# Performance work log

Hardware: AMD Instinct MI355X
Metric: run time of the kernel (lower is better)

The kernel has to match this reference:

```python
import jax, jax.numpy as jnp
import numpy as np
import math

D_MODEL = 1024
N_HEADS = 16
D_K = D_MODEL // N_HEADS
ROPE_BASE = 10000.0


def rope_cos_sin(seq_len, d_k, base=ROPE_BASE, dtype=jnp.float32):
    inv_freq = 1.0 / base ** (jnp.arange(0, d_k, 2, dtype=dtype) / d_k)  # [d_k/2]
    pos = jnp.arange(seq_len, dtype=dtype)
    freqs = jnp.outer(pos, inv_freq)  # [T, d_k/2]
    return jnp.cos(freqs), jnp.sin(freqs)


def apply_rope(x, cos, sin):
    # x: [B, H, T, d_k]; cos/sin: [T, d_k/2]
    x1 = x[..., 0::2]
    x2 = x[..., 1::2]
    c = cos[None, None]
    s = sin[None, None]
    r1 = x1 * c - x2 * s
    r2 = x1 * s + x2 * c
    return jnp.stack([r1, r2], axis=-1).reshape(x.shape)


def setup_inputs() -> dict:
    key = jax.random.key(0)
    ks = jax.random.split(key, 7)
    B, T = 2, 2048
    scale = 1.0 / math.sqrt(D_MODEL)
    return {
        "query": jax.random.normal(ks[0], (B, T, D_MODEL), jnp.float32),
        "key": jax.random.normal(ks[1], (B, T, D_MODEL), jnp.float32),
        "value": jax.random.normal(ks[2], (B, T, D_MODEL), jnp.float32),
        "Wq": jax.random.normal(ks[3], (D_MODEL, D_MODEL), jnp.float32) * scale,
        "Wk": jax.random.normal(ks[4], (D_MODEL, D_MODEL), jnp.float32) * scale,
        "Wv": jax.random.normal(ks[5], (D_MODEL, D_MODEL), jnp.float32) * scale,
        "Wo": jax.random.normal(ks[6], (D_MODEL, D_MODEL), jnp.float32) * scale,
    }


def reference(query, key, value, Wq, Wk, Wv, Wo):
    B, Tq, _ = query.shape
    Tk = key.shape[1]
    # nn.Linear: x @ W.T
    Q = (query @ Wq.T).reshape(B, Tq, N_HEADS, D_K).transpose(0, 2, 1, 3)
    K = (key @ Wk.T).reshape(B, Tk, N_HEADS, D_K).transpose(0, 2, 1, 3)
    V = (value @ Wv.T).reshape(B, Tk, N_HEADS, D_K).transpose(0, 2, 1, 3)
    cos_q, sin_q = rope_cos_sin(Tq, D_K)
    cos_k, sin_k = rope_cos_sin(Tk, D_K)
    Q = apply_rope(Q, cos_q, sin_q)
    K = apply_rope(K, cos_k, sin_k)
    scores = jnp.einsum("bhqd,bhkd->bhqk", Q, K) / math.sqrt(D_K)
    attn = jax.nn.softmax(scores, axis=-1)
    out = jnp.einsum("bhqk,bhkd->bhqd", attn, V)
    out = out.transpose(0, 2, 1, 3).reshape(B, Tq, D_MODEL)
    return out @ Wo.T
```

## Files before the change

### kernel.cpp

```cpp
#include <hip/hip_runtime.h>
#include <hip/hip_bf16.h>
#include <cstdint>

typedef unsigned short u16;
typedef __attribute__((ext_vector_type(4))) float fl4;
typedef __attribute__((ext_vector_type(2))) float fl2;
typedef __attribute__((ext_vector_type(4))) unsigned short u16x4;
typedef __attribute__((ext_vector_type(8))) unsigned short u16x8;
typedef __attribute__((ext_vector_type(2))) unsigned int u32x2;
typedef __attribute__((ext_vector_type(8))) __bf16 bf16x8;
typedef __attribute__((ext_vector_type(4))) float f32x4;

#define MKE 4194304
#define NKE 1048576

static __device__ __forceinline__ u16 f2bf(float x) {
  unsigned int u = __builtin_bit_cast(unsigned int, x);
  u += 0x7fffu + ((u >> 16) & 1u);
  return (u16)(u >> 16);
}

static __device__ __forceinline__ unsigned int cvtpk(float a, float b) {
  unsigned int r;
  asm("v_cvt_pk_bf16_f32 %0, %1, %2" : "=v"(r) : "v"(a), "v"(b));
  return r;
}

static __device__ __forceinline__ f32x4 mfma16(bf16x8 a, bf16x8 b, f32x4 c) {
  return __builtin_amdgcn_mfma_f32_16x16x32_bf16(a, b, c, 0, 0, 0);
}

static __device__ __forceinline__ void gload_lds16(const void* g, void* l) {
  __builtin_amdgcn_global_load_lds((const __attribute__((address_space(1))) void*)g,
                                   (__attribute__((address_space(3))) void*)l,
                                   16, 0, 0);
}

__global__ __launch_bounds__(256) void k_prep(const float* __restrict__ q,
                                              const float* __restrict__ k,
                                              const float* __restrict__ v,
                                              const float* __restrict__ wq,
                                              const float* __restrict__ wk,
                                              const float* __restrict__ wv,
                                              const float* __restrict__ wo,
                                              u16* __restrict__ ws,
                                              float* __restrict__ tab) {
  const int bid = blockIdx.x;
  if (bid >= 16384) {
    const int idx = (bid - 16384) * 256 + threadIdx.x;
    const int t = idx >> 5, i = idx & 31;
    const float ang = (float)t * exp2f(-0.4152410118609203f * (float)i);
    float sn, cs;
    sincosf(ang, &sn, &cs);
    reinterpret_cast<fl2*>(tab)[idx] = (fl2){cs, sn};
    return;
  }
  const int i = bid * 256 + threadIdx.x;
  const float* src;
  u16* dst;
  int loc;
  if (i < 3 * 1048576) {
    const int seg = i >> 20;
    loc = i & 1048575;
    src = seg == 0 ? q : (seg == 1 ? k : v);
    dst = ws + (size_t)seg * MKE;
  } else {
    const int j = i - 3 * 1048576;
    const int seg = j >> 18;
    loc = j & 262143;
    src = seg == 0 ? wq : (seg == 1 ? wk : (seg == 2 ? wv : wo));
    dst = ws + 3 * (size_t)MKE + (size_t)seg * NKE;
  }
  fl4 val = reinterpret_cast<const fl4*>(src)[loc];
  u16x4 o;
  o[0] = f2bf(val[0]); o[1] = f2bf(val[1]); o[2] = f2bf(val[2]); o[3] = f2bf(val[3]);
  reinterpret_cast<u16x4*>(dst)[loc] = o;
}

__global__ __launch_bounds__(256) void k_gemm_qkv(
    const u16* __restrict__ aq, const u16* __restrict__ ak, const u16* __restrict__ av,
    const u16* __restrict__ bq, const u16* __restrict__ bk, const u16* __restrict__ bv,
    u16* __restrict__ cq, u16* __restrict__ ck, u16* __restrict__ cv,
    const fl2* __restrict__ tab) {
  constexpr int K = 1024;
  __shared__ __align__(16) u16 smem[16384];
  u16* sA = smem;
  u16* sB = smem + 8192;
  const int z = blockIdx.z;
  const u16* A  = z == 0 ? aq : (z == 1 ? ak : av);
  const u16* Bw = z == 0 ? bq : (z == 1 ? bk : bv);
  u16* C        = z == 0 ? cq : (z == 1 ? ck : cv);
  const float scale = (z == 0) ? 0.18033688011112042f : 1.0f;

  const int tid = threadIdx.x;
  const int w = tid >> 6, lane = tid & 63;
  const int wm = w >> 1, wn = w & 1;
  const int trow = blockIdx.y << 7, tcol = blockIdx.x << 7;
  const int l15 = lane & 15, l4 = lane >> 4;
  const int srow = lane >> 3;
  const int scol = ((lane & 7) ^ srow) << 3;

  f32x4 acc[4][4];
#pragma unroll
  for (int m = 0; m < 4; ++m)
#pragma unroll
    for (int n = 0; n < 4; ++n) acc[m][n] = (f32x4){0.f, 0.f, 0.f, 0.f};

  for (int k0 = 0; k0 < K; k0 += 64) {
#pragma unroll
    for (int c = 0; c < 4; ++c) {
      const int g = c * 4 + w;
      const int row = g * 8 + srow;
      gload_lds16(A + (size_t)(trow + row) * K + (k0 + scol), (void*)(sA + g * 512));
      gload_lds16(Bw + (size_t)(tcol + row) * K + (k0 + scol), (void*)(sB + g * 512));
    }
    __syncthreads();
#pragma unroll
    for (int kc = 0; kc < 2; ++kc) {
      const int kb = (kc * 32 + l4 * 8) * 2;
      bf16x8 af[4], bfr[4];
#pragma unroll
      for (int m = 0; m < 4; ++m) {
        const int r = wm * 64 + m * 16 + l15;
        af[m] = *reinterpret_cast<const bf16x8*>(
            reinterpret_cast<const char*>(sA) + r * 128 + (kb ^ ((r & 7) << 4)));
      }
#pragma unroll
      for (int n = 0; n < 4; ++n) {
        const int r = wn * 64 + n * 16 + l15;
        bfr[n] = *reinterpret_cast<const bf16x8*>(
            reinterpret_cast<const char*>(sB) + r * 128 + (kb ^ ((r & 7) << 4)));
      }
      __builtin_amdgcn_s_setprio(1);
#pragma unroll
      for (int m = 0; m < 4; ++m)
#pragma unroll
        for (int n = 0; n < 4; ++n)
          acc[m][n] = mfma16(af[m], bfr[n], acc[m][n]);
      __builtin_amdgcn_s_setprio(0);
    }
    __syncthreads();
  }

  if (z < 2) {
#pragma unroll
    for (int m = 0; m < 4; ++m) {
#pragma unroll
      for (int n = 0; n < 4; ++n) {
#pragma unroll
        for (int r = 0; r < 4; ++r) {
          const float vsc = acc[m][n][r] * scale;
          const int row = trow + wm * 64 + m * 16 + l4 * 4 + r;
          const int col = tcol + wn * 64 + n * 16 + l15;
          const int b = row >> 11, t = row & 2047;
          const int h = col >> 6, d = col & 63;
          const float partner = __shfl_xor(vsc, 1);
          const fl2 cs = tab[t * 32 + (d >> 1)];
          const float outv =
              (d & 1) ? (partner * cs.y + vsc * cs.x) : (vsc * cs.x - partner * cs.y);
          C[((size_t)((b << 4) + h) * 2048 + t) * 64 + d] = f2bf(outv);
        }
      }
    }
  } else {
#pragma unroll
    for (int m = 0; m < 4; ++m)
#pragma unroll
      for (int n = 0; n < 4; ++n)
#pragma unroll
        for (int r = 0; r < 4; ++r) {
          const int c = wn * 64 + n * 16 + l15;
          const int rl = wm * 64 + m * 16 + l4 * 4 + r;
          smem[c * 128 + (rl ^ ((c & 15) * 8))] = f2bf(acc[m][n][r]);
        }
    __syncthreads();
    const int bq = trow >> 11;
    const int tb = trow & 2047;
#pragma unroll
    for (int j = 0; j < 8; ++j) {
      const int flat = (tid + j * 256) * 8;
      const int c = flat >> 7, r0 = flat & 127;
      u16x8 vv = *reinterpret_cast<const u16x8*>(smem + c * 128 + (r0 ^ ((c & 15) * 8)));
      const int col = tcol + c;
      u16* dst = C + ((size_t)((bq << 4) + (col >> 6)) * 64 + (col & 63)) * 2048 + tb + r0;
      *reinterpret_cast<u16x8*>(dst) = vv;
    }
  }
}

__global__ __launch_bounds__(256) void k_gemm_o(const u16* __restrict__ A,
                                                const u16* __restrict__ Bw,
                                                float* __restrict__ C) {
  constexpr int K = 1024, N = 1024;
  __shared__ __align__(16) u16 sA[2][128 * 64];
  __shared__ __align__(16) u16 sB[2][64 * 64];
  const int tid = threadIdx.x;
  const int w = tid >> 6, lane = tid & 63;
  const int wm = w >> 1, wn = w & 1;
  const int trow = blockIdx.y << 7, tcol = blockIdx.x << 6;
  const int l15 = lane & 15, l4 = lane >> 4;
  const int srow = lane >> 3;
  const int scol = ((lane & 7) ^ srow) << 3;

  f32x4 acc[4][2];
#pragma unroll
  for (int m = 0; m < 4; ++m)
#pragma unroll
    for (int n = 0; n < 2; ++n) acc[m][n] = (f32x4){0.f, 0.f, 0.f, 0.f};

  auto stage = [&](int k0, int buf) {
#pragma unroll
    for (int c = 0; c < 4; ++c) {
      const int g = c * 4 + w;
      const int row = g * 8 + srow;
      gload_lds16(A + (size_t)(trow + row) * K + (k0 + scol), (void*)(sA[buf] + g * 512));
    }
#pragma unroll
    for (int c = 0; c < 2; ++c) {
      const int g = c * 4 + w;
      const int row = g * 8 + srow;
      gload_lds16(Bw + (size_t)(tcol + row) * K + (k0 + scol), (void*)(sB[buf] + g * 512));
    }
  };

  stage(0, 0);
  __syncthreads();

  for (int t = 0; t < 16; ++t) {
    const int buf = t & 1;
    if (t + 1 < 16) stage((t + 1) * 64, buf ^ 1);
#pragma unroll
    for (int kc = 0; kc < 2; ++kc) {
      const int kb = (kc * 32 + l4 * 8) * 2;
      bf16x8 af[4], bfr[2];
#pragma unroll
      for (int m = 0; m < 4; ++m) {
        const int r = wm * 64 + m * 16 + l15;
        af[m] = *reinterpret_cast<const bf16x8*>(
            reinterpret_cast<const char*>(sA[buf]) + r * 128 + (kb ^ ((r & 7) << 4)));
      }
#pragma unroll
      for (int n = 0; n < 2; ++n) {
        const int r = wn * 32 + n * 16 + l15;
        bfr[n] = *reinterpret_cast<const bf16x8*>(
            reinterpret_cast<const char*>(sB[buf]) + r * 128 + (kb ^ ((r & 7) << 4)));
      }
      __builtin_amdgcn_s_setprio(1);
#pragma unroll
      for (int m = 0; m < 4; ++m)
#pragma unroll
        for (int n = 0; n < 2; ++n)
          acc[m][n] = mfma16(af[m], bfr[n], acc[m][n]);
      __builtin_amdgcn_s_setprio(0);
    }
    __syncthreads();
  }

#pragma unroll
  for (int m = 0; m < 4; ++m)
#pragma unroll
    for (int n = 0; n < 2; ++n)
#pragma unroll
      for (int r = 0; r < 4; ++r) {
        const int row = trow + wm * 64 + m * 16 + l4 * 4 + r;
        const int col = tcol + wn * 32 + n * 16 + l15;
        C[(size_t)row * N + col] = acc[m][n][r];
      }
}

__global__ __launch_bounds__(256) void k_attn(const u16* __restrict__ Q,
                                              const u16* __restrict__ Kh,
                                              const u16* __restrict__ Vt,
                                              u16* __restrict__ Oout) {
  __shared__ __align__(16) char lds[40960];
  const int tid = threadIdx.x;
  const int w = tid >> 6, lane = tid & 63;
  const int l15 = lane & 15, l4 = lane >> 4;
  const int nb = blockIdx.x;
  const int xcd = nb & 7, idx = nb >> 3;
  const int bh = xcd * 4 + (idx >> 5);
  const int q0 = (idx & 31) << 6;

  const u16* Qg = Q + (size_t)bh * (2048 * 64);
  const u16* Kg = Kh + (size_t)bh * (2048 * 64);
  const u16* Vg = Vt + (size_t)bh * (64 * 2048);

  const int swz = (l15 & 7) << 4;
  const int rk0 = l15 * 128 + ((l4 * 16) ^ swz);
  const int rk1 = rk0 ^ 64;
  const int pbase = 32768 + w * 2048 + l15 * 128;
  int pwv[4];
#pragma unroll
  for (int nn = 0; nn < 4; ++nn) pwv[nn] = pbase + (((nn * 32) | (l4 * 8)) ^ swz);
  const int rp0 = pbase + ((l4 * 16) ^ swz);
  const int rp1 = rp0 ^ 64;
  const int wst = w * 1024;

  const int srow8 = lane >> 3;
  const int scol = ((lane & 7) ^ srow8) << 3;
  const u16* gK0 = Kg + (size_t)(w * 8 + srow8) * 64 + scol;
  const u16* gK1 = gK0 + 2048;
  const u16* gV0 = Vg + (size_t)(w * 8 + srow8) * 2048 + scol;
  const u16* gV1 = gV0 + 65536;

  bf16x8 qf0, qf1;
  {
    const u16* qp = Qg + (size_t)(q0 + w * 16 + l15) * 64 + l4 * 8;
    qf0 = *reinterpret_cast<const bf16x8*>(qp);
    qf1 = *reinterpret_cast<const bf16x8*>(qp + 32);
  }

  f32x4 o[4];
#pragma unroll
  for (int nn = 0; nn < 4; ++nn) o[nn] = (f32x4){0.f, 0.f, 0.f, 0.f};
  float lrun = 0.f;

  gload_lds16(gK0, lds + wst);
  gload_lds16(gK1, lds + wst + 4096);
  gload_lds16(gV0, lds + 16384 + wst);
  gload_lds16(gV1, lds + 16384 + wst + 4096);
  gK0 += 4096; gK1 += 4096; gV0 += 64; gV1 += 64;
  __syncthreads();

#define ATTN_STEP(BUFOFF, PREF, POFF)                                            \
  {                                                                              \
    if (PREF) {                                                                  \
      gload_lds16(gK0, lds + (POFF) + wst);                                      \
      gload_lds16(gK1, lds + (POFF) + wst + 4096);                               \
      gload_lds16(gV0, lds + 16384 + (POFF) + wst);                              \
      gload_lds16(gV1, lds + 16384 + (POFF) + wst + 4096);                       \
      gK0 += 4096; gK1 += 4096; gV0 += 64; gV1 += 64;                            \
    }                                                                            \
    f32x4 s[4];                                                                  \
    s[0] = (f32x4){0.f, 0.f, 0.f, 0.f}; s[1] = (f32x4){0.f, 0.f, 0.f, 0.f};      \
    s[2] = (f32x4){0.f, 0.f, 0.f, 0.f}; s[3] = (f32x4){0.f, 0.f, 0.f, 0.f};      \
    __builtin_amdgcn_s_setprio(1);                                               \
    _Pragma("unroll")                                                            \
    for (int nn = 0; nn < 4; ++nn) {                                             \
      bf16x8 kf = *(const bf16x8*)(lds + (BUFOFF) + rk0 + nn * 2048);            \
      s[nn] = mfma16(kf, qf0, s[nn]);                                            \
    }                                                                            \
    _Pragma("unroll")                                                            \
    for (int nn = 0; nn < 4; ++nn) {                                             \
      bf16x8 kf = *(const bf16x8*)(lds + (BUFOFF) + rk1 + nn * 2048);            \
      s[nn] = mfma16(kf, qf1, s[nn]);                                            \
    }                                                                            \
    __builtin_amdgcn_s_setprio(0);                                               \
    float pp[4][4];                                                              \
    _Pragma("unroll")                                                            \
    for (int nn = 0; nn < 4; ++nn) {                                             \
      pp[nn][0] = __builtin_amdgcn_exp2f(s[nn][0]);                              \
      pp[nn][1] = __builtin_amdgcn_exp2f(s[nn][1]);                              \
      pp[nn][2] = __builtin_amdgcn_exp2f(s[nn][2]);                              \
      pp[nn][3] = __builtin_amdgcn_exp2f(s[nn][3]);                              \
    }                                                                            \
    _Pragma("unroll")                                                            \
    for (int nn = 0; nn < 4; ++nn) {                                             \
      u32x2 pk;                                                                  \
      pk[0] = cvtpk(pp[nn][0], pp[nn][1]);                                       \
      pk[1] = cvtpk(pp[nn][2], pp[nn][3]);                                       \
      *(u32x2*)(lds + pwv[nn]) = pk;                                             \
    }                                                                            \
    float rs = ((pp[0][0] + pp[0][1]) + (pp[0][2] + pp[0][3])) +                 \
               ((pp[1][0] + pp[1][1]) + (pp[1][2] + pp[1][3])) +                 \
               ((pp[2][0] + pp[2][1]) + (pp[2][2] + pp[2][3])) +                 \
               ((pp[3][0] + pp[3][1]) + (pp[3][2] + pp[3][3]));                  \
    rs += __shfl_xor(rs, 16);                                                    \
    rs += __shfl_xor(rs, 32);                                                    \
    lrun += rs;                                                                  \
    __builtin_amdgcn_s_setprio(1);                                               \
    _Pragma("unroll")                                                            \
    for (int kc = 0; kc < 2; ++kc) {                                             \
      const bf16x8 pf = *(const bf16x8*)(lds + (kc ? rp1 : rp0));                \
      const int rkk = kc ? rk1 : rk0;                                            \
      _Pragma("unroll")                                                          \
      for (int nn = 0; nn < 4; ++nn) {                                           \
        bf16x8 vf = *(const bf16x8*)(lds + 16384 + (BUFOFF) + rkk + nn * 2048);  \
        o[nn] = mfma16(pf, vf, o[nn]);                                           \
      }                                                                          \
    }                                                                            \
    __builtin_amdgcn_s_setprio(0);                                               \
    __syncthreads();                                                             \
  }

  for (int cc = 0; cc < 16; ++cc) {
    ATTN_STEP(0, 1, 8192)
    ATTN_STEP(8192, (cc != 15), 0)
  }
#undef ATTN_STEP

  const int b = bh >> 4, h = bh & 15;
  float lr[4];
#pragma unroll
  for (int r = 0; r < 4; ++r)
    lr[r] = 1.f / __shfl(lrun, (lane & 48) | (l4 * 4 + r));
#pragma unroll
  for (int nn = 0; nn < 4; ++nn)
#pragma unroll
    for (int r = 0; r < 4; ++r) {
      const int t = q0 + w * 16 + l4 * 4 + r;
      const int d = nn * 16 + l15;
      Oout[((size_t)(b * 2048 + t)) * 1024 + h * 64 + d] = f2bf(o[nn][r] * lr[r]);
    }
}

extern "C" void kernel_launch(void* const* d_in, const int* in_sizes, int n_in,
                              void* d_out, int out_size, void* d_ws, size_t ws_size,
                              hipStream_t stream) {
  const float* q  = (const float*)d_in[0];
  const float* k  = (const float*)d_in[1];
  const float* v  = (const float*)d_in[2];
  const float* wq = (const float*)d_in[3];
  const float* wk = (const float*)d_in[4];
  const float* wv = (const float*)d_in[5];
  const float* wo = (const float*)d_in[6];

  u16* ws = (u16*)d_ws;
  u16* Xq  = ws;
  u16* Xk  = Xq + MKE;
  u16* Xv  = Xk + MKE;
  u16* Wqb = Xv + MKE;
  u16* Wkb = Wqb + NKE;
  u16* Wvb = Wkb + NKE;
  u16* Wob = Wvb + NKE;
  u16* Qr  = Wob + NKE;
  u16* Kr  = Qr + MKE;
  u16* Vtm = Kr + MKE;
  u16* Vtr = Vtm + MKE;
  u16* AO  = Vtr + MKE;
  float* tab = (float*)AO;

  k_prep<<<16640, 256, 0, stream>>>(q, k, v, wq, wk, wv, wo, ws, tab);
  k_gemm_qkv<<<dim3(8, 32, 3), 256, 0, stream>>>(Xq, Xk, Xv, Wqb, Wkb, Wvb,
                                                 Qr, Kr, Vtr, (const fl2*)tab);
  k_attn<<<1024, 256, 0, stream>>>(Qr, Kr, Vtr, AO);
  k_gemm_o<<<dim3(16, 32), 256, 0, stream>>>(AO, Wob, (float*)d_out);
}
```

Measured before the change: 135.9 us.

## Process two 16-row query tiles per wave in attention kernel

```diff
diff --git a/kernel.cpp b/kernel.cpp
--- a/kernel.cpp
+++ b/kernel.cpp
@@ -272,14 +272,14 @@
                                               const u16* __restrict__ Kh,
                                               const u16* __restrict__ Vt,
                                               u16* __restrict__ Oout) {
-  __shared__ __align__(16) char lds[40960];
+  __shared__ __align__(16) char lds[49152];
   const int tid = threadIdx.x;
   const int w = tid >> 6, lane = tid & 63;
   const int l15 = lane & 15, l4 = lane >> 4;
   const int nb = blockIdx.x;
   const int xcd = nb & 7, idx = nb >> 3;
-  const int bh = xcd * 4 + (idx >> 5);
-  const int q0 = (idx & 31) << 6;
+  const int bh = xcd * 4 + (idx >> 4);
+  const int q0 = (idx & 15) << 7;
 
   const u16* Qg = Q + (size_t)bh * (2048 * 64);
   const u16* Kg = Kh + (size_t)bh * (2048 * 64);
@@ -288,12 +288,12 @@
   const int swz = (l15 & 7) << 4;
   const int rk0 = l15 * 128 + ((l4 * 16) ^ swz);
   const int rk1 = rk0 ^ 64;
-  const int pbase = 32768 + w * 2048 + l15 * 128;
-  int pwv[4];
-#pragma unroll
-  for (int nn = 0; nn < 4; ++nn) pwv[nn] = pbase + (((nn * 32) | (l4 * 8)) ^ swz);
-  const int rp0 = pbase + ((l4 * 16) ^ swz);
-  const int rp1 = rp0 ^ 64;
+  const int pbase = 32768 + w * 4096 + l15 * 128;
+  int pwvA[4];
+#pragma unroll
+  for (int nn = 0; nn < 4; ++nn) pwvA[nn] = pbase + (((nn * 32) | (l4 * 8)) ^ swz);
+  const int rpA0 = pbase + ((l4 * 16) ^ swz);
+  const int rpA1 = rpA0 ^ 64;
   const int wst = w * 1024;
 
   const int srow8 = lane >> 3;
@@ -303,17 +303,23 @@
   const u16* gV0 = Vg + (size_t)(w * 8 + srow8) * 2048 + scol;
   const u16* gV1 = gV0 + 65536;
 
-  bf16x8 qf0, qf1;
+  bf16x8 qf0, qf1, qf2, qf3;
   {
-    const u16* qp = Qg + (size_t)(q0 + w * 16 + l15) * 64 + l4 * 8;
-    qf0 = *reinterpret_cast<const bf16x8*>(qp);
-    qf1 = *reinterpret_cast<const bf16x8*>(qp + 32);
-  }
-
-  f32x4 o[4];
-#pragma unroll
-  for (int nn = 0; nn < 4; ++nn) o[nn] = (f32x4){0.f, 0.f, 0.f, 0.f};
-  float lrun = 0.f;
+    const u16* qpA = Qg + (size_t)(q0 + w * 32 + l15) * 64 + l4 * 8;
+    qf0 = *reinterpret_cast<const bf16x8*>(qpA);
+    qf1 = *reinterpret_cast<const bf16x8*>(qpA + 32);
+    const u16* qpB = qpA + 16 * 64;
+    qf2 = *reinterpret_cast<const bf16x8*>(qpB);
+    qf3 = *reinterpret_cast<const bf16x8*>(qpB + 32);
+  }
+
+  f32x4 oA[4], oB[4];
+#pragma unroll
+  for (int nn = 0; nn < 4; ++nn) {
+    oA[nn] = (f32x4){0.f, 0.f, 0.f, 0.f};
+    oB[nn] = (f32x4){0.f, 0.f, 0.f, 0.f};
+  }
+  float lrunA = 0.f, lrunB = 0.f;
 
   gload_lds16(gK0, lds + wst);
   gload_lds16(gK1, lds + wst + 4096);
@@ -331,52 +337,68 @@
       gload_lds16(gV1, lds + 16384 + (POFF) + wst + 4096);                       \
       gK0 += 4096; gK1 += 4096; gV0 += 64; gV1 += 64;                            \
     }                                                                            \
-    f32x4 s[4];                                                                  \
-    s[0] = (f32x4){0.f, 0.f, 0.f, 0.f}; s[1] = (f32x4){0.f, 0.f, 0.f, 0.f};      \
-    s[2] = (f32x4){0.f, 0.f, 0.f, 0.f}; s[3] = (f32x4){0.f, 0.f, 0.f, 0.f};      \
+    f32x4 sA[4], sB[4];                                                          \
     __builtin_amdgcn_s_setprio(1);                                               \
     _Pragma("unroll")                                                            \
     for (int nn = 0; nn < 4; ++nn) {                                             \
       bf16x8 kf = *(const bf16x8*)(lds + (BUFOFF) + rk0 + nn * 2048);            \
-      s[nn] = mfma16(kf, qf0, s[nn]);                                            \
+      sA[nn] = mfma16(kf, qf0, (f32x4){0.f, 0.f, 0.f, 0.f});                     \
+      sB[nn] = mfma16(kf, qf2, (f32x4){0.f, 0.f, 0.f, 0.f});                     \
     }                                                                            \
     _Pragma("unroll")                                                            \
     for (int nn = 0; nn < 4; ++nn) {                                             \
       bf16x8 kf = *(const bf16x8*)(lds + (BUFOFF) + rk1 + nn * 2048);            \
-      s[nn] = mfma16(kf, qf1, s[nn]);                                            \
+      sA[nn] = mfma16(kf, qf1, sA[nn]);                                          \
+      sB[nn] = mfma16(kf, qf3, sB[nn]);                                          \
     }                                                                            \
     __builtin_amdgcn_s_setprio(0);                                               \
-    float pp[4][4];                                                              \
+    float ppA[4][4], ppB[4][4];                                                  \
     _Pragma("unroll")                                                            \
     for (int nn = 0; nn < 4; ++nn) {                                             \
-      pp[nn][0] = __builtin_amdgcn_exp2f(s[nn][0]);                              \
-      pp[nn][1] = __builtin_amdgcn_exp2f(s[nn][1]);                              \
-      pp[nn][2] = __builtin_amdgcn_exp2f(s[nn][2]);                              \
-      pp[nn][3] = __builtin_amdgcn_exp2f(s[nn][3]);                              \
+      ppA[nn][0] = __builtin_amdgcn_exp2f(sA[nn][0]);                            \
+      ppA[nn][1] = __builtin_amdgcn_exp2f(sA[nn][1]);                            \
+      ppA[nn][2] = __builtin_amdgcn_exp2f(sA[nn][2]);                            \
+      ppA[nn][3] = __builtin_amdgcn_exp2f(sA[nn][3]);                            \
+      ppB[nn][0] = __builtin_amdgcn_exp2f(sB[nn][0]);                            \
+      ppB[nn][1] = __builtin_amdgcn_exp2f(sB[nn][1]);                            \
+      ppB[nn][2] = __builtin_amdgcn_exp2f(sB[nn][2]);                            \
+      ppB[nn][3] = __builtin_amdgcn_exp2f(sB[nn][3]);                            \
     }                                                                            \
     _Pragma("unroll")                                                            \
     for (int nn = 0; nn < 4; ++nn) {                                             \
-      u32x2 pk;                                                                  \
-      pk[0] = cvtpk(pp[nn][0], pp[nn][1]);                                       \
-      pk[1] = cvtpk(pp[nn][2], pp[nn][3]);                                       \
-      *(u32x2*)(lds + pwv[nn]) = pk;                                             \
-    }                                                                            \
-    float rs = ((pp[0][0] + pp[0][1]) + (pp[0][2] + pp[0][3])) +                 \
-               ((pp[1][0] + pp[1][1]) + (pp[1][2] + pp[1][3])) +                 \
-               ((pp[2][0] + pp[2][1]) + (pp[2][2] + pp[2][3])) +                 \
-               ((pp[3][0] + pp[3][1]) + (pp[3][2] + pp[3][3]));                  \
-    rs += __shfl_xor(rs, 16);                                                    \
-    rs += __shfl_xor(rs, 32);                                                    \
-    lrun += rs;                                                                  \
+      u32x2 pkA, pkB;                                                            \
+      pkA[0] = cvtpk(ppA[nn][0], ppA[nn][1]);                                    \
+      pkA[1] = cvtpk(ppA[nn][2], ppA[nn][3]);                                    \
+      pkB[0] = cvtpk(ppB[nn][0], ppB[nn][1]);                                    \
+      pkB[1] = cvtpk(ppB[nn][2], ppB[nn][3]);                                    \
+      *(u32x2*)(lds + pwvA[nn]) = pkA;                                           \
+      *(u32x2*)(lds + pwvA[nn] + 2048) = pkB;                                    \
+    }                                                                            \
+    float rsA = ((ppA[0][0] + ppA[0][1]) + (ppA[0][2] + ppA[0][3])) +            \
+                ((ppA[1][0] + ppA[1][1]) + (ppA[1][2] + ppA[1][3])) +            \
+                ((ppA[2][0] + ppA[2][1]) + (ppA[2][2] + ppA[2][3])) +            \
+                ((ppA[3][0] + ppA[3][1]) + (ppA[3][2] + ppA[3][3]));             \
+    float rsB = ((ppB[0][0] + ppB[0][1]) + (ppB[0][2] + ppB[0][3])) +            \
+                ((ppB[1][0] + ppB[1][1]) + (ppB[1][2] + ppB[1][3])) +            \
+                ((ppB[2][0] + ppB[2][1]) + (ppB[2][2] + ppB[2][3])) +            \
+                ((ppB[3][0] + ppB[3][1]) + (ppB[3][2] + ppB[3][3]));             \
+    rsA += __shfl_xor(rsA, 16);                                                  \
+    rsA += __shfl_xor(rsA, 32);                                                  \
+    rsB += __shfl_xor(rsB, 16);                                                  \
+    rsB += __shfl_xor(rsB, 32);                                                  \
+    lrunA += rsA;                                                                \
+    lrunB += rsB;                                                                \
     __builtin_amdgcn_s_setprio(1);                                               \
     _Pragma("unroll")                                                            \
     for (int kc = 0; kc < 2; ++kc) {                                             \
-      const bf16x8 pf = *(const bf16x8*)(lds + (kc ? rp1 : rp0));                \
+      const bf16x8 pfA = *(const bf16x8*)(lds + (kc ? rpA1 : rpA0));             \
+      const bf16x8 pfB = *(const bf16x8*)(lds + (kc ? rpA1 : rpA0) + 2048);      \
       const int rkk = kc ? rk1 : rk0;                                            \
       _Pragma("unroll")                                                          \
       for (int nn = 0; nn < 4; ++nn) {                                           \
         bf16x8 vf = *(const bf16x8*)(lds + 16384 + (BUFOFF) + rkk + nn * 2048);  \
-        o[nn] = mfma16(pf, vf, o[nn]);                                           \
+        oA[nn] = mfma16(pfA, vf, oA[nn]);                                        \
+        oB[nn] = mfma16(pfB, vf, oB[nn]);                                        \
       }                                                                          \
     }                                                                            \
     __builtin_amdgcn_s_setprio(0);                                               \
@@ -390,17 +412,21 @@
 #undef ATTN_STEP
 
   const int b = bh >> 4, h = bh & 15;
-  float lr[4];
-#pragma unroll
-  for (int r = 0; r < 4; ++r)
-    lr[r] = 1.f / __shfl(lrun, (lane & 48) | (l4 * 4 + r));
+  float lrA[4], lrB[4];
+#pragma unroll
+  for (int r = 0; r < 4; ++r) {
+    const int src = (lane & 48) | (l4 * 4 + r);
+    lrA[r] = 1.f / __shfl(lrunA, src);
+    lrB[r] = 1.f / __shfl(lrunB, src);
+  }
 #pragma unroll
   for (int nn = 0; nn < 4; ++nn)
 #pragma unroll
     for (int r = 0; r < 4; ++r) {
-      const int t = q0 + w * 16 + l4 * 4 + r;
+      const int tA = q0 + w * 32 + l4 * 4 + r;
       const int d = nn * 16 + l15;
-      Oout[((size_t)(b * 2048 + t)) * 1024 + h * 64 + d] = f2bf(o[nn][r] * lr[r]);
+      Oout[((size_t)(b * 2048 + tA)) * 1024 + h * 64 + d] = f2bf(oA[nn][r] * lrA[r]);
+      Oout[((size_t)(b * 2048 + tA + 16)) * 1024 + h * 64 + d] = f2bf(oB[nn][r] * lrB[r]);
     }
 }
 
@@ -433,6 +459,6 @@
   k_prep<<<16640, 256, 0, stream>>>(q, k, v, wq, wk, wv, wo, ws, tab);
   k_gemm_qkv<<<dim3(8, 32, 3), 256, 0, stream>>>(Xq, Xk, Xv, Wqb, Wkb, Wvb,
                                                  Qr, Kr, Vtr, (const fl2*)tab);
-  k_attn<<<1024, 256, 0, stream>>>(Qr, Kr, Vtr, AO);
+  k_attn<<<512, 256, 0, stream>>>(Qr, Kr, Vtr, AO);
   k_gemm_o<<<dim3(16, 32), 256, 0, stream>>>(AO, Wob, (float*)d_out);
 }
```

After: 129.9 us. 1.05x faster.
